# Performance work log

Hardware: AMD Instinct MI355X
Metric: run time of the kernel (lower is better)

## Reference

```python
import jax, jax.numpy as jnp
import numpy as np
from jax import lax

N, C_IN, C_OUT, T, V = 16, 256, 256, 300, 25
K = 3            # s_kernel_size
TK = 9           # t_kernel_size
BN_EPS = 1e-5


def setup_inputs() -> dict:
    key = jax.random.key(0)
    ks = jax.random.split(key, 12)
    x = jax.random.normal(ks[0], (N, C_IN, T, V), dtype=jnp.float32)
    A = jax.random.uniform(ks[1], (K, V, V), dtype=jnp.float32)
    att_A = jax.random.uniform(ks[2], (N, 1, V, V), dtype=jnp.float32)  # unused by S_GC
    M = jnp.ones((K, V, V), dtype=jnp.float32)
    # 1x1 spatial conv: out = K*C_OUT channels
    conv_w = jax.random.normal(ks[3], (K * C_OUT, C_IN), dtype=jnp.float32) * 0.02
    conv_b = jnp.zeros((K * C_OUT,), dtype=jnp.float32)
    # BN1 (eval mode)
    bn1_gamma = jnp.ones((C_OUT,), dtype=jnp.float32)
    bn1_beta = jnp.zeros((C_OUT,), dtype=jnp.float32)
    bn1_mean = jax.random.normal(ks[4], (C_OUT,), dtype=jnp.float32) * 0.1
    bn1_var = jax.random.uniform(ks[5], (C_OUT,), dtype=jnp.float32) + 0.5
    # temporal conv: kernel (TK, 1), stride 1, pad ((TK-1)//2, 0)
    tconv_w = jax.random.normal(ks[6], (C_OUT, C_OUT, TK, 1), dtype=jnp.float32) * 0.02
    tconv_b = jnp.zeros((C_OUT,), dtype=jnp.float32)
    # BN2 (eval mode)
    bn2_gamma = jnp.ones((C_OUT,), dtype=jnp.float32)
    bn2_beta = jnp.zeros((C_OUT,), dtype=jnp.float32)
    bn2_mean = jax.random.normal(ks[7], (C_OUT,), dtype=jnp.float32) * 0.1
    bn2_var = jax.random.uniform(ks[8], (C_OUT,), dtype=jnp.float32) + 0.5
    return {
        "x": x, "A": A, "att_A": att_A, "M": M,
        "conv_w": conv_w, "conv_b": conv_b,
        "bn1_gamma": bn1_gamma, "bn1_beta": bn1_beta, "bn1_mean": bn1_mean, "bn1_var": bn1_var,
        "tconv_w": tconv_w, "tconv_b": tconv_b,
        "bn2_gamma": bn2_gamma, "bn2_beta": bn2_beta, "bn2_mean": bn2_mean, "bn2_var": bn2_var,
    }


def _bn(x, gamma, beta, mean, var):
    # eval-mode BatchNorm2d over channel dim of NCHW tensor
    scale = gamma / jnp.sqrt(var + BN_EPS)
    return x * scale[None, :, None, None] + (beta - mean * scale)[None, :, None, None]


def reference(x, A, att_A, M, conv_w, conv_b,
              bn1_gamma, bn1_beta, bn1_mean, bn1_var,
              tconv_w, tconv_b,
              bn2_gamma, bn2_beta, bn2_mean, bn2_var):
    # --- S_GC: 1x1 conv -> view (n,K,c,t,v) -> einsum with A*M ---
    y = jnp.einsum('nctv,oc->notv', x, conv_w) + conv_b[None, :, None, None]
    y = y.reshape(N, K, C_OUT, T, V)
    sgc = jnp.einsum('nkctv,kvw->nctw', y, A * M)
    # --- tgc: BN -> ReLU -> temporal conv -> BN -> Dropout(0) -> ReLU ---
    h = jax.nn.relu(_bn(sgc, bn1_gamma, bn1_beta, bn1_mean, bn1_var))
    h = lax.conv_general_dilated(
        h, tconv_w, window_strides=(1, 1),
        padding=(((TK - 1) // 2, (TK - 1) // 2), (0, 0)),
        dimension_numbers=('NCHW', 'OIHW', 'NCHW'))
    h = h + tconv_b[None, :, None, None]
    h = jax.nn.relu(_bn(h, bn2_gamma, bn2_beta, bn2_mean, bn2_var))
    # --- residual: identity (in_channels == out_channels, stride == 1) ---
    return h + x
```

## Files before the change

### kernel.cpp

```cpp
#include <hip/hip_runtime.h>
#include <math.h>

constexpr int TVL = 7500;
constexpr int CIN = 256;
constexpr int CO  = 256;
constexpr int KO  = 768;
constexpr int KK3 = 2304;
#define BNEPS 1e-5f

typedef __attribute__((ext_vector_type(8))) short short8;
typedef __attribute__((ext_vector_type(4))) float f32x4;
typedef unsigned short ushortT;

static __device__ __forceinline__ ushortT f2bf(float v) {
    unsigned x = __float_as_uint(v);
    unsigned r = (x + 0x7fffu + ((x >> 16) & 1u)) >> 16;
    return (ushortT)r;
}
static __device__ __forceinline__ float bf2f(ushortT u) {
    return __uint_as_float((unsigned)u << 16);
}

static __device__ __forceinline__ void gll16(const void* g, void* l) {
    __builtin_amdgcn_global_load_lds(
        (const __attribute__((address_space(1))) void*)g,
        (__attribute__((address_space(3))) void*)l, 16, 0, 0);
}

static __device__ __forceinline__ void xcd_remap(int gx, int gy,
                                                 int& bx, int& by, int& bz)
{
    const int gz = gridDim.z;
    const int total = gx * gy * gz;
    const int lin = blockIdx.x + gx * (blockIdx.y + gy * blockIdx.z);
    const int q = total >> 3, r = total & 7;
    const int xcd = lin & 7, idx = lin >> 3;
    const int nl = (xcd < r ? xcd * (q + 1) : r * (q + 1) + (xcd - r) * q) + idx;
    bx = nl % gx;
    const int rest = nl / gx;
    by = rest % gy;
    bz = rest / gy;
}

__global__ void ksplit_w1(const float* __restrict__ w,
                          ushortT* __restrict__ dH, ushortT* __restrict__ dL,
                          ushortT* __restrict__ zb)
{
    if (blockIdx.x == 0 && threadIdx.x < 128) zb[threadIdx.x] = 0;
    int i = blockIdx.x * 256 + threadIdx.x;
    if (i < KO * CIN) {
        float v = w[i];
        ushortT h = f2bf(v);
        dH[i] = h;
        dL[i] = f2bf(v - bf2f(h));
    }
}

__global__ void ksplit_w3(const float* __restrict__ w,
                          ushortT* __restrict__ dH, ushortT* __restrict__ dL)
{
    int i = blockIdx.x * 256 + threadIdx.x;
    if (i < CO * KK3) {
        int o = i / KK3, rem = i - o * KK3;
        int c = rem / 9, dt = rem - c * 9;
        float v = w[i];
        ushortT h = f2bf(v);
        int j = o * KK3 + dt * 256 + c;
        dH[j] = h;
        dL[j] = f2bf(v - bf2f(h));
    }
}

__global__ __launch_bounds__(256) void ktrans_split(
    const float* __restrict__ src, size_t zstr,
    ushortT* __restrict__ dH, ushortT* __restrict__ dL)
{
    __shared__ float tile[32][33];
    const int z = blockIdx.z;
    src += (size_t)z * zstr;
    dH  += (size_t)z * TVL * 256;
    dL  += (size_t)z * TVL * 256;
    const int tx = threadIdx.x & 31, ty = threadIdx.x >> 5;
    const int wBase = blockIdx.x * 32, cBase = blockIdx.y * 32;
    #pragma unroll
    for (int i = 0; i < 4; ++i) {
        int r = ty + i * 8;
        int w = wBase + tx;
        tile[r][tx] = (w < TVL) ? src[(size_t)(cBase + r) * TVL + w] : 0.f;
    }
    __syncthreads();
    #pragma unroll
    for (int i = 0; i < 4; ++i) {
        int wr = ty + i * 8;
        int w = wBase + wr;
        if (w < TVL) {
            float v = tile[tx][wr];
            ushortT hi = f2bf(v);
            ushortT lo = f2bf(v - bf2f(hi));
            dH[(size_t)w * 256 + cBase + tx] = hi;
            dL[(size_t)w * 256 + cBase + tx] = lo;
        }
    }
}

__global__ __launch_bounds__(256) void k1_mfma(
    const ushortT* __restrict__ Wh, const ushortT* __restrict__ Wl,
    const ushortT* __restrict__ Xh, const ushortT* __restrict__ Xl,
    const ushortT* __restrict__ zb,
    const float* __restrict__ bias, float* __restrict__ out1)
{
    __shared__ __align__(16) short Ah[2][4096], Al[2][4096], Bh[2][4096], Bl[2][4096];
    const int tid = threadIdx.x;
    int bx, by, bz;
    xcd_remap(gridDim.x, gridDim.y, bx, by, bz);
    const int ng = bz;
    const int rowBase = by * 128;
    const int colBase = bx * 128;
    const ushortT* XhN = Xh + (size_t)ng * TVL * 256;
    const ushortT* XlN = Xl + (size_t)ng * TVL * 256;

    f32x4 acc[4][4];
    #pragma unroll
    for (int a = 0; a < 4; ++a)
        #pragma unroll
        for (int b = 0; b < 4; ++b) acc[a][b] = (f32x4){0.f, 0.f, 0.f, 0.f};

    const int r0 = tid >> 2, s = tid & 3;
    const int wv = tid >> 6, lane = tid & 63;
    const int wy = wv >> 1, wx = wv & 1;
    const int q = lane >> 4, l15 = lane & 15;
    const int qs0 = s ^ ((r0 >> 1) & 3);
    const int qsr = q ^ ((l15 >> 1) & 3);
    const int ldo0 = tid * 16, ldo1 = 4096 + tid * 16;
    const int bcol0 = colBase + r0, bcol1 = colBase + r0 + 64;

    auto stage = [&](int kk, int p) {
        short* ahp = Ah[p]; short* alp = Al[p];
        short* bhp = Bh[p]; short* blp = Bl[p];
        const size_t goA = (size_t)(rowBase + r0) * CIN + kk + qs0 * 8;
        gll16(Wh + goA, (char*)ahp + ldo0);
        gll16(Wl + goA, (char*)alp + ldo0);
        gll16(Wh + goA + (size_t)64 * CIN, (char*)ahp + ldo1);
        gll16(Wl + goA + (size_t)64 * CIN, (char*)alp + ldo1);
        const size_t goB0 = (size_t)bcol0 * 256 + kk + qs0 * 8;
        const size_t goB1 = (size_t)bcol1 * 256 + kk + qs0 * 8;
        gll16(bcol0 < TVL ? (const void*)(XhN + goB0) : (const void*)zb, (char*)bhp + ldo0);
        gll16(bcol0 < TVL ? (const void*)(XlN + goB0) : (const void*)zb, (char*)blp + ldo0);
        gll16(bcol1 < TVL ? (const void*)(XhN + goB1) : (const void*)zb, (char*)bhp + ldo1);
        gll16(bcol1 < TVL ? (const void*)(XlN + goB1) : (const void*)zb, (char*)blp + ldo1);
    };

    stage(0, 0);
    __syncthreads();
    int p = 0;

    #pragma unroll 1
    for (int kk = 0; kk < CIN; kk += 32) {
        if (kk + 32 < CIN) stage(kk + 32, p ^ 1);

        const char* AhP = (const char*)Ah[p];
        const char* AlP = (const char*)Al[p];
        const char* BhP = (const char*)Bh[p];
        const char* BlP = (const char*)Bl[p];
        short8 ah[4], al[4], bh[4], bl[4];
        #pragma unroll
        for (int mi = 0; mi < 4; ++mi) {
            const int off = (wy * 64 + mi * 16 + l15) * 64 + qsr * 16;
            ah[mi] = *(const short8*)(AhP + off);
            al[mi] = *(const short8*)(AlP + off);
        }
        #pragma unroll
        for (int ni = 0; ni < 4; ++ni) {
            const int off = (wx * 64 + ni * 16 + l15) * 64 + qsr * 16;
            bh[ni] = *(const short8*)(BhP + off);
            bl[ni] = *(const short8*)(BlP + off);
        }
        #pragma unroll
        for (int mi = 0; mi < 4; ++mi)
            #pragma unroll
            for (int ni = 0; ni < 4; ++ni) {
                acc[mi][ni] = __builtin_amdgcn_mfma_f32_16x16x32_bf16(ah[mi], bh[ni], acc[mi][ni], 0, 0, 0);
                acc[mi][ni] = __builtin_amdgcn_mfma_f32_16x16x32_bf16(ah[mi], bl[ni], acc[mi][ni], 0, 0, 0);
                acc[mi][ni] = __builtin_amdgcn_mfma_f32_16x16x32_bf16(al[mi], bh[ni], acc[mi][ni], 0, 0, 0);
            }
        __syncthreads();
        p ^= 1;
    }

    float* out1n = out1 + (size_t)ng * KO * TVL;
    #pragma unroll
    for (int mi = 0; mi < 4; ++mi)
        #pragma unroll
        for (int rr = 0; rr < 4; ++rr) {
            const int row = rowBase + wy * 64 + mi * 16 + q * 4 + rr;
            const float bv = bias[row];
            #pragma unroll
            for (int ni = 0; ni < 4; ++ni) {
                const int col = colBase + wx * 64 + ni * 16 + l15;
                if (col < TVL)
                    out1n[(size_t)row * TVL + col] = acc[mi][ni][rr] + bv;
            }
        }
}

__global__ __launch_bounds__(256) void k2_sgc(
    const float* out1, const float* __restrict__ A,
    const float* __restrict__ Mm, const float* __restrict__ g1,
    const float* __restrict__ b1, const float* __restrict__ m1,
    const float* __restrict__ v1, float* h)
{
    __shared__ __align__(16) float AMs[3 * 25 * 28];
    const int tid = threadIdx.x;
    for (int i = tid; i < 1875; i += 256)
        AMs[(i / 25) * 28 + (i % 25)] = A[i] * Mm[i];
    __syncthreads();

    const int r  = blockIdx.x * 256 + tid;
    const int t2 = r % 150;
    const int rc = r / 150;
    const int c  = rc & 255;
    const int ng = rc >> 8;
    const int t  = t2 * 2;

    const float* base = out1 + ((size_t)ng * KO + c) * TVL + t * 25;
    float o0[25], o1[25];
    #pragma unroll
    for (int w = 0; w < 25; ++w) { o0[w] = 0.f; o1[w] = 0.f; }

    for (int k = 0; k < 3; ++k) {
        const float* yp = base + (size_t)k * CO * TVL;
        float y0[25], y1[25];
        #pragma unroll
        for (int v = 0; v < 25; ++v) { y0[v] = yp[v]; y1[v] = yp[25 + v]; }
        const float* amk = &AMs[k * 25 * 28];
        for (int v = 0; v < 25; ++v) {
            const float* am = amk + v * 28;
            const float ya = y0[v], yb = y1[v];
            #pragma unroll
            for (int w = 0; w < 25; ++w) {
                const float a = am[w];
                o0[w] += ya * a;
                o1[w] += yb * a;
            }
        }
    }

    const float sc = g1[c] / sqrtf(v1[c] + BNEPS);
    const float bi = b1[c] - m1[c] * sc;
    float* hp = h + ((size_t)ng * KO + c) * TVL + t * 25;
    #pragma unroll
    for (int w = 0; w < 25; ++w) {
        const float va = o0[w] * sc + bi;
        const float vb = o1[w] * sc + bi;
        hp[w]      = va > 0.f ? va : 0.f;
        hp[25 + w] = vb > 0.f ? vb : 0.f;
    }
}

__global__ __launch_bounds__(256) void k3_mfma(
    const ushortT* __restrict__ Wh, const ushortT* __restrict__ Wl,
    const ushortT* __restrict__ Hh, const ushortT* __restrict__ Hl,
    const ushortT* __restrict__ zb,
    const float* __restrict__ tb, const float* __restrict__ g2,
    const float* __restrict__ b2, const float* __restrict__ m2,
    const float* __restrict__ v2, const float* __restrict__ x,
    float* __restrict__ out, int n0)
{
    __shared__ __align__(16) short Sh[384 * 32], Sl[384 * 32];
    __shared__ __align__(16) short Ah[2][4096], Al[2][4096];
    const int tid = threadIdx.x;
    int bx, by, bz;
    xcd_remap(gridDim.x, gridDim.y, bx, by, bz);
    const int ng = bz;
    const int rowBase = by * 128;
    const int colBase = bx * 128;
    const ushortT* HhN = Hh + (size_t)ng * TVL * 256;
    const ushortT* HlN = Hl + (size_t)ng * TVL * 256;

    f32x4 acc[4][4];
    #pragma unroll
    for (int a = 0; a < 4; ++a)
        #pragma unroll
        for (int b = 0; b < 4; ++b) acc[a][b] = (f32x4){0.f, 0.f, 0.f, 0.f};

    const int r0 = tid >> 2, s = tid & 3;
    const int wv = tid >> 6, lane = tid & 63;
    const int wy = wv >> 1, wx = wv & 1;
    const int q = lane >> 4, l15 = lane & 15;
    const int qs0 = s ^ ((r0 >> 1) & 3);
    const int qsr = q ^ ((l15 >> 1) & 3);
    const int ldo0 = tid * 16, ldo1 = 4096 + tid * 16;

    auto stageStrip = [&](int c0) {
        #pragma unroll
        for (int i = 0; i < 6; ++i) {
            const int gcol = colBase - 128 + i * 64 + r0;
            const bool ok = (unsigned)gcol < (unsigned)TVL;
            const size_t go = (size_t)gcol * 256 + c0 + qs0 * 8;
            gll16(ok ? (const void*)(HhN + go) : (const void*)zb,
                  (char*)Sh + i * 4096 + tid * 16);
            gll16(ok ? (const void*)(HlN + go) : (const void*)zb,
                  (char*)Sl + i * 4096 + tid * 16);
        }
    };
    auto stageA = [&](int kp, int p) {
        short* ahp = Ah[p]; short* alp = Al[p];
        const size_t goA = (size_t)(rowBase + r0) * KK3 + kp + qs0 * 8;
        gll16(Wh + goA, (char*)ahp + ldo0);
        gll16(Wl + goA, (char*)alp + ldo0);
        gll16(Wh + goA + (size_t)64 * KK3, (char*)ahp + ldo1);
        gll16(Wl + goA + (size_t)64 * KK3, (char*)alp + ldo1);
    };

    stageA(0, 0);
    int p = 0;

    #pragma unroll 1
    for (int cc = 0; cc < 8; ++cc) {
        const int c0 = cc * 32;
        stageStrip(c0);
        __syncthreads();

        #pragma unroll 1
        for (int dt = 0; dt < 9; ++dt) {
            {
                int ndt = dt + 1, nc0 = c0;
                if (ndt == 9) { ndt = 0; nc0 += 32; }
                if (nc0 < 256) stageA(ndt * 256 + nc0, p ^ 1);
            }

            const char* AhP = (const char*)Ah[p];
            const char* AlP = (const char*)Al[p];
            short8 ah[4], al[4], bh[4], bl[4];
            #pragma unroll
            for (int mi = 0; mi < 4; ++mi) {
                const int off = (wy * 64 + mi * 16 + l15) * 64 + qsr * 16;
                ah[mi] = *(const short8*)(AhP + off);
                al[mi] = *(const short8*)(AlP + off);
            }
            const int sbase = wx * 64 + dt * 25 + 28;
            #pragma unroll
            for (int ni = 0; ni < 4; ++ni) {
                const int sc = sbase + ni * 16 + l15;
                const int off = sc * 64 + ((q ^ ((sc >> 1) & 3)) << 4);
                bh[ni] = *(const short8*)((const char*)Sh + off);
                bl[ni] = *(const short8*)((const char*)Sl + off);
            }
            #pragma unroll
            for (int mi = 0; mi < 4; ++mi)
                #pragma unroll
                for (int ni = 0; ni < 4; ++ni) {
                    acc[mi][ni] = __builtin_amdgcn_mfma_f32_16x16x32_bf16(ah[mi], bh[ni], acc[mi][ni], 0, 0, 0);
                    acc[mi][ni] = __builtin_amdgcn_mfma_f32_16x16x32_bf16(ah[mi], bl[ni], acc[mi][ni], 0, 0, 0);
                    acc[mi][ni] = __builtin_amdgcn_mfma_f32_16x16x32_bf16(al[mi], bh[ni], acc[mi][ni], 0, 0, 0);
                }
            __syncthreads();
            p ^= 1;
        }
    }

    const float* xn = x   + (size_t)(n0 + ng) * CO * TVL;
    float*       on = out + (size_t)(n0 + ng) * CO * TVL;
    #pragma unroll
    for (int mi = 0; mi < 4; ++mi)
        #pragma unroll
        for (int rr = 0; rr < 4; ++rr) {
            const int row = rowBase + wy * 64 + mi * 16 + q * 4 + rr;
            const float sc = g2[row] / sqrtf(v2[row] + BNEPS);
            const float bb = (tb[row] - m2[row]) * sc + b2[row];
            #pragma unroll
            for (int ni = 0; ni < 4; ++ni) {
                const int col = colBase + wx * 64 + ni * 16 + l15;
                if (col < TVL) {
                    const size_t o = (size_t)row * TVL + col;
                    on[o] = fmaxf(acc[mi][ni][rr] * sc + bb, 0.f) + xn[o];
                }
            }
        }
}

extern "C" void kernel_launch(void* const* d_in, const int* in_sizes, int n_in,
                              void* d_out, int out_size, void* d_ws, size_t ws_size,
                              hipStream_t stream)
{
    const float* x  = (const float*)d_in[0];
    const float* A  = (const float*)d_in[1];
    const float* Mm = (const float*)d_in[3];
    const float* cw = (const float*)d_in[4];
    const float* cb = (const float*)d_in[5];
    const float* g1 = (const float*)d_in[6];
    const float* b1 = (const float*)d_in[7];
    const float* m1 = (const float*)d_in[8];
    const float* v1 = (const float*)d_in[9];
    const float* tw = (const float*)d_in[10];
    const float* tb = (const float*)d_in[11];
    const float* g2 = (const float*)d_in[12];
    const float* b2 = (const float*)d_in[13];
    const float* m2 = (const float*)d_in[14];
    const float* v2 = (const float*)d_in[15];
    float* out = (float*)d_out;

    ushortT* zb  = (ushortT*)d_ws;
    ushortT* W1h = (ushortT*)((char*)d_ws + 256);
    ushortT* W1l = W1h + KO * CIN;
    ushortT* W3h = W1l + KO * CIN;
    ushortT* W3l = W3h + CO * KK3;
    char* dyn = (char*)(W3l + CO * KK3);
    const size_t fixed = (size_t)(dyn - (char*)d_ws);
    const size_t avail = ws_size > fixed ? ws_size - fixed : 0;
    const size_t perN = (size_t)KO * TVL * 4 + 2 * (size_t)TVL * 256 * 2;
    int g = 16;
    while (g > 1 && (size_t)g * perN > avail) g >>= 1;

    float*   out1 = (float*)dyn;
    ushortT* Xh   = (ushortT*)(out1 + (size_t)g * KO * TVL);
    ushortT* Xl   = Xh + (size_t)g * TVL * 256;

    hipLaunchKernelGGL(ksplit_w1, dim3((KO * CIN + 255) / 256), dim3(256), 0, stream, cw, W1h, W1l, zb);
    hipLaunchKernelGGL(ksplit_w3, dim3((CO * KK3 + 255) / 256), dim3(256), 0, stream, tw, W3h, W3l);

    for (int n0 = 0; n0 < 16; n0 += g) {
        hipLaunchKernelGGL(ktrans_split, dim3(235, 8, g), dim3(256), 0, stream,
                           x + (size_t)n0 * CIN * TVL, (size_t)CIN * TVL, Xh, Xl);
        hipLaunchKernelGGL(k1_mfma, dim3(59, 6, g), dim3(256), 0, stream,
                           W1h, W1l, Xh, Xl, zb, cb, out1);
        hipLaunchKernelGGL(k2_sgc, dim3(g * 150), dim3(256), 0, stream,
                           out1, A, Mm, g1, b1, m1, v1, out1 );
        hipLaunchKernelGGL(ktrans_split, dim3(235, 8, g), dim3(256), 0, stream,
                           out1, (size_t)KO * TVL, Xh, Xl);
        hipLaunchKernelGGL(k3_mfma, dim3(59, 2, g), dim3(256), 0, stream,
                           W3h, W3l, Xh, Xl, zb, tb, g2, b2, m2, v2, x, out, n0);
    }
}
```

Baseline: 1.206 ms.

## Load weight fragments directly into registers instead of LDS staging in MFMA GEMMs

Both MFMA GEMM kernels now skip staging the weight (A) tiles through shared memory and instead prefetch each wave's A fragments straight from global memory into registers, double-buffered one step ahead. This removes the A-side LDS traffic and, in the temporal-conv kernel, the per-tap barrier, leaving only a barrier around each strip restage. The B fragment loads are interleaved with the MFMAs, and launch bounds request 3 blocks per SM. The trade-off is more register pressure and uncoalesced global loads of weights repeated across blocks, relying on cache hits.

```diff
diff --git a/kernel.cpp b/kernel.cpp
--- a/kernel.cpp
+++ b/kernel.cpp
@@ -103,13 +103,13 @@
     }
 }
 
-__global__ __launch_bounds__(256) void k1_mfma(
+__global__ __launch_bounds__(256, 3) void k1_mfma(
     const ushortT* __restrict__ Wh, const ushortT* __restrict__ Wl,
     const ushortT* __restrict__ Xh, const ushortT* __restrict__ Xl,
     const ushortT* __restrict__ zb,
     const float* __restrict__ bias, float* __restrict__ out1)
 {
-    __shared__ __align__(16) short Ah[2][4096], Al[2][4096], Bh[2][4096], Bl[2][4096];
+    __shared__ __align__(16) short Bh[2][4096], Bl[2][4096];
     const int tid = threadIdx.x;
     int bx, by, bz;
     xcd_remap(gridDim.x, gridDim.y, bx, by, bz);
@@ -130,18 +130,14 @@
     const int wy = wv >> 1, wx = wv & 1;
     const int q = lane >> 4, l15 = lane & 15;
     const int qs0 = s ^ ((r0 >> 1) & 3);
-    const int qsr = q ^ ((l15 >> 1) & 3);
     const int ldo0 = tid * 16, ldo1 = 4096 + tid * 16;
     const int bcol0 = colBase + r0, bcol1 = colBase + r0 + 64;
 
-    auto stage = [&](int kk, int p) {
-        short* ahp = Ah[p]; short* alp = Al[p];
+    const ushortT* WhR = Wh + (size_t)(rowBase + wy * 64 + l15) * CIN + q * 8;
+    const ushortT* WlR = Wl + (size_t)(rowBase + wy * 64 + l15) * CIN + q * 8;
+
+    auto stageB = [&](int kk, int p) {
         short* bhp = Bh[p]; short* blp = Bl[p];
-        const size_t goA = (size_t)(rowBase + r0) * CIN + kk + qs0 * 8;
-        gll16(Wh + goA, (char*)ahp + ldo0);
-        gll16(Wl + goA, (char*)alp + ldo0);
-        gll16(Wh + goA + (size_t)64 * CIN, (char*)ahp + ldo1);
-        gll16(Wl + goA + (size_t)64 * CIN, (char*)alp + ldo1);
         const size_t goB0 = (size_t)bcol0 * 256 + kk + qs0 * 8;
         const size_t goB1 = (size_t)bcol1 * 256 + kk + qs0 * 8;
         gll16(bcol0 < TVL ? (const void*)(XhN + goB0) : (const void*)zb, (char*)bhp + ldo0);
@@ -149,42 +145,49 @@
         gll16(bcol1 < TVL ? (const void*)(XhN + goB1) : (const void*)zb, (char*)bhp + ldo1);
         gll16(bcol1 < TVL ? (const void*)(XlN + goB1) : (const void*)zb, (char*)blp + ldo1);
     };
-
-    stage(0, 0);
+    auto loadA = [&](int kk, short8* dh, short8* dl) {
+        #pragma unroll
+        for (int mi = 0; mi < 4; ++mi) {
+            dh[mi] = *(const short8*)(WhR + (size_t)mi * 16 * CIN + kk);
+            dl[mi] = *(const short8*)(WlR + (size_t)mi * 16 * CIN + kk);
+        }
+    };
+
+    short8 cAh[4], cAl[4], nAh[4], nAl[4];
+    loadA(0, cAh, cAl);
+    stageB(0, 0);
     __syncthreads();
     int p = 0;
 
     #pragma unroll 1
     for (int kk = 0; kk < CIN; kk += 32) {
-        if (kk + 32 < CIN) stage(kk + 32, p ^ 1);
-
-        const char* AhP = (const char*)Ah[p];
-        const char* AlP = (const char*)Al[p];
+        const bool more = (kk + 32 < CIN);
+        if (more) {
+            loadA(kk + 32, nAh, nAl);
+            stageB(kk + 32, p ^ 1);
+        }
+
         const char* BhP = (const char*)Bh[p];
         const char* BlP = (const char*)Bl[p];
-        short8 ah[4], al[4], bh[4], bl[4];
-        #pragma unroll
-        for (int mi = 0; mi < 4; ++mi) {
-            const int off = (wy * 64 + mi * 16 + l15) * 64 + qsr * 16;
-            ah[mi] = *(const short8*)(AhP + off);
-            al[mi] = *(const short8*)(AlP + off);
-        }
         #pragma unroll
         for (int ni = 0; ni < 4; ++ni) {
-            const int off = (wx * 64 + ni * 16 + l15) * 64 + qsr * 16;
-            bh[ni] = *(const short8*)(BhP + off);
-            bl[ni] = *(const short8*)(BlP + off);
-        }
-        #pragma unroll
-        for (int mi = 0; mi < 4; ++mi)
-            #pragma unroll
-            for (int ni = 0; ni < 4; ++ni) {
-                acc[mi][ni] = __builtin_amdgcn_mfma_f32_16x16x32_bf16(ah[mi], bh[ni], acc[mi][ni], 0, 0, 0);
-                acc[mi][ni] = __builtin_amdgcn_mfma_f32_16x16x32_bf16(ah[mi], bl[ni], acc[mi][ni], 0, 0, 0);
-                acc[mi][ni] = __builtin_amdgcn_mfma_f32_16x16x32_bf16(al[mi], bh[ni], acc[mi][ni], 0, 0, 0);
-            }
+            const int scn = wx * 64 + ni * 16 + l15;
+            const int off = scn * 64 + ((q ^ ((scn >> 1) & 3)) << 4);
+            const short8 bh = *(const short8*)(BhP + off);
+            const short8 bl = *(const short8*)(BlP + off);
+            #pragma unroll
+            for (int mi = 0; mi < 4; ++mi) {
+                acc[mi][ni] = __builtin_amdgcn_mfma_f32_16x16x32_bf16(cAh[mi], bh, acc[mi][ni], 0, 0, 0);
+                acc[mi][ni] = __builtin_amdgcn_mfma_f32_16x16x32_bf16(cAh[mi], bl, acc[mi][ni], 0, 0, 0);
+                acc[mi][ni] = __builtin_amdgcn_mfma_f32_16x16x32_bf16(cAl[mi], bh, acc[mi][ni], 0, 0, 0);
+            }
+        }
         __syncthreads();
         p ^= 1;
+        if (more) {
+            #pragma unroll
+            for (int i = 0; i < 4; ++i) { cAh[i] = nAh[i]; cAl[i] = nAl[i]; }
+        }
     }
 
     float* out1n = out1 + (size_t)ng * KO * TVL;
@@ -257,7 +260,7 @@
     }
 }
 
-__global__ __launch_bounds__(256) void k3_mfma(
+__global__ __launch_bounds__(256, 3) void k3_mfma(
     const ushortT* __restrict__ Wh, const ushortT* __restrict__ Wl,
     const ushortT* __restrict__ Hh, const ushortT* __restrict__ Hl,
     const ushortT* __restrict__ zb,
@@ -267,7 +270,6 @@
     float* __restrict__ out, int n0)
 {
     __shared__ __align__(16) short Sh[384 * 32], Sl[384 * 32];
-    __shared__ __align__(16) short Ah[2][4096], Al[2][4096];
     const int tid = threadIdx.x;
     int bx, by, bz;
     xcd_remap(gridDim.x, gridDim.y, bx, by, bz);
@@ -288,8 +290,9 @@
     const int wy = wv >> 1, wx = wv & 1;
     const int q = lane >> 4, l15 = lane & 15;
     const int qs0 = s ^ ((r0 >> 1) & 3);
-    const int qsr = q ^ ((l15 >> 1) & 3);
-    const int ldo0 = tid * 16, ldo1 = 4096 + tid * 16;
+
+    const ushortT* WhR = Wh + (size_t)(rowBase + wy * 64 + l15) * KK3 + q * 8;
+    const ushortT* WlR = Wl + (size_t)(rowBase + wy * 64 + l15) * KK3 + q * 8;
 
     auto stageStrip = [&](int c0) {
         #pragma unroll
@@ -303,59 +306,49 @@
                   (char*)Sl + i * 4096 + tid * 16);
         }
     };
-    auto stageA = [&](int kp, int p) {
-        short* ahp = Ah[p]; short* alp = Al[p];
-        const size_t goA = (size_t)(rowBase + r0) * KK3 + kp + qs0 * 8;
-        gll16(Wh + goA, (char*)ahp + ldo0);
-        gll16(Wl + goA, (char*)alp + ldo0);
-        gll16(Wh + goA + (size_t)64 * KK3, (char*)ahp + ldo1);
-        gll16(Wl + goA + (size_t)64 * KK3, (char*)alp + ldo1);
+    auto loadA = [&](int kp, short8* dh, short8* dl) {
+        #pragma unroll
+        for (int mi = 0; mi < 4; ++mi) {
+            dh[mi] = *(const short8*)(WhR + (size_t)mi * 16 * KK3 + kp);
+            dl[mi] = *(const short8*)(WlR + (size_t)mi * 16 * KK3 + kp);
+        }
     };
 
-    stageA(0, 0);
-    int p = 0;
+    short8 cAh[4], cAl[4], nAh[4], nAl[4];
+    loadA(0, cAh, cAl);
 
     #pragma unroll 1
     for (int cc = 0; cc < 8; ++cc) {
         const int c0 = cc * 32;
+        if (cc) __syncthreads();
         stageStrip(c0);
         __syncthreads();
 
         #pragma unroll 1
         for (int dt = 0; dt < 9; ++dt) {
-            {
-                int ndt = dt + 1, nc0 = c0;
-                if (ndt == 9) { ndt = 0; nc0 += 32; }
-                if (nc0 < 256) stageA(ndt * 256 + nc0, p ^ 1);
-            }
-
-            const char* AhP = (const char*)Ah[p];
-            const char* AlP = (const char*)Al[p];
-            short8 ah[4], al[4], bh[4], bl[4];
-            #pragma unroll
-            for (int mi = 0; mi < 4; ++mi) {
-                const int off = (wy * 64 + mi * 16 + l15) * 64 + qsr * 16;
-                ah[mi] = *(const short8*)(AhP + off);
-                al[mi] = *(const short8*)(AlP + off);
-            }
+            int ndt = dt + 1, nc0 = c0;
+            if (ndt == 9) { ndt = 0; nc0 += 32; }
+            const bool hasNext = (nc0 < 256);
+            if (hasNext) loadA(ndt * 256 + nc0, nAh, nAl);
+
             const int sbase = wx * 64 + dt * 25 + 28;
             #pragma unroll
             for (int ni = 0; ni < 4; ++ni) {
                 const int sc = sbase + ni * 16 + l15;
                 const int off = sc * 64 + ((q ^ ((sc >> 1) & 3)) << 4);
-                bh[ni] = *(const short8*)((const char*)Sh + off);
-                bl[ni] = *(const short8*)((const char*)Sl + off);
-            }
-            #pragma unroll
-            for (int mi = 0; mi < 4; ++mi)
+                const short8 bh = *(const short8*)((const char*)Sh + off);
+                const short8 bl = *(const short8*)((const char*)Sl + off);
                 #pragma unroll
-                for (int ni = 0; ni < 4; ++ni) {
-                    acc[mi][ni] = __builtin_amdgcn_mfma_f32_16x16x32_bf16(ah[mi], bh[ni], acc[mi][ni], 0, 0, 0);
-                    acc[mi][ni] = __builtin_amdgcn_mfma_f32_16x16x32_bf16(ah[mi], bl[ni], acc[mi][ni], 0, 0, 0);
-                    acc[mi][ni] = __builtin_amdgcn_mfma_f32_16x16x32_bf16(al[mi], bh[ni], acc[mi][ni], 0, 0, 0);
+                for (int mi = 0; mi < 4; ++mi) {
+                    acc[mi][ni] = __builtin_amdgcn_mfma_f32_16x16x32_bf16(cAh[mi], bh, acc[mi][ni], 0, 0, 0);
+                    acc[mi][ni] = __builtin_amdgcn_mfma_f32_16x16x32_bf16(cAh[mi], bl, acc[mi][ni], 0, 0, 0);
+                    acc[mi][ni] = __builtin_amdgcn_mfma_f32_16x16x32_bf16(cAl[mi], bh, acc[mi][ni], 0, 0, 0);
                 }
-            __syncthreads();
-            p ^= 1;
+            }
+            if (hasNext) {
+                #pragma unroll
+                for (int i = 0; i < 4; ++i) { cAh[i] = nAh[i]; cAl[i] = nAl[i]; }
+            }
         }
     }
 
```

New measurement: 1.435 ms. 19.0% more time.
